# Kernel optimization log

Measured on AMD Instinct MI355X. Metric: run time of the kernel, lower is better.

## Reference

```python
import jax, jax.numpy as jnp
import numpy as np

D_MODEL = 1024
N_HEADS = 16
FEATURE_DIM = 16
HEAD_DIM = D_MODEL // N_HEADS  # 64
EPS = 1e-12


def taylor_exp(x):
    """2nd-order Taylor feature map of exp(q^T k / sqrt(d)).
    x: (b, h, l, d) -> (b, h, l, 1 + d + d^2)"""
    d = x.shape[-1]
    rd = jnp.sqrt(jnp.asarray(d, x.dtype))      # sqrt(d)
    rrd = jnp.sqrt(rd)                          # d^(1/4)
    r2 = jnp.sqrt(jnp.asarray(2.0, x.dtype))
    x2 = (x[..., :, None] * x[..., None, :]).reshape(*x.shape[:-1], d * d) / r2
    ones = jnp.ones_like(x[..., :1])
    return jnp.concatenate([ones, x / rrd, x2 / rd], axis=-1)


def setup_inputs() -> dict:
    key = jax.random.key(0)
    k0, k1, k2, k3, k4 = jax.random.split(key, 5)
    b, l = 1, 1024
    scale = 1.0 / np.sqrt(D_MODEL)
    hidden_states = jax.random.normal(k0, (b, l, D_MODEL), dtype=jnp.float32)
    Wq = jax.random.normal(k1, (N_HEADS * FEATURE_DIM, D_MODEL), dtype=jnp.float32) * scale
    Wk = jax.random.normal(k2, (N_HEADS * FEATURE_DIM, D_MODEL), dtype=jnp.float32) * scale
    Wv = jax.random.normal(k3, (N_HEADS * HEAD_DIM, D_MODEL), dtype=jnp.float32) * scale
    Wo = jax.random.normal(k4, (D_MODEL, N_HEADS * HEAD_DIM), dtype=jnp.float32) * scale
    return {"hidden_states": hidden_states, "Wq": Wq, "Wk": Wk, "Wv": Wv, "Wo": Wo}


def reference(hidden_states, Wq, Wk, Wv, Wo):
    b, l, _ = hidden_states.shape
    # projections (bias-free)
    q = (hidden_states @ Wq.T).reshape(b, l, N_HEADS, FEATURE_DIM).transpose(0, 2, 1, 3)
    k = (hidden_states @ Wk.T).reshape(b, l, N_HEADS, FEATURE_DIM).transpose(0, 2, 1, 3)
    v = (hidden_states @ Wv.T).reshape(b, l, N_HEADS, HEAD_DIM).transpose(0, 2, 1, 3)
    qf = taylor_exp(q)   # (b, h, l, D) with D = 1 + d + d^2 = 273
    kf = taylor_exp(k)
    # causal linear attention via associative KV accumulation
    # kv_state[l] = sum_{t<=l} phi(k_t) outer v_t  -> (b, h, l, head_dim, D)
    kv_state = jnp.cumsum(kf[..., None, :] * v[..., :, None], axis=2)
    num = jnp.einsum('bhlD,bhldD->bhld', qf, kv_state)
    den = jnp.einsum('bhlD,bhlD->bhl', qf, jnp.cumsum(kf, axis=2))[..., None] + EPS
    y = num / den                                # (b, h, l, head_dim)
    y = y.transpose(0, 2, 1, 3).reshape(b, l, N_HEADS * HEAD_DIM)
    return y @ Wo.T
```

## Files before the change

### kernel.cpp

```cpp
#include <hip/hip_runtime.h>

#define LSEQ 1024
#define DMODEL 1024
#define NHEADS 16
#define FDIM 16
#define HDIM 64
#define CHUNK 64
#define NCHUNK 16

typedef __attribute__((ext_vector_type(8))) short short8;
typedef __attribute__((ext_vector_type(4))) float floatx4;

__device__ __forceinline__ float bf2f(unsigned short u) {
    unsigned int x = ((unsigned int)u) << 16;
    return __builtin_bit_cast(float, x);
}
__device__ __forceinline__ unsigned short f2bf(float f) {
    unsigned int x = __builtin_bit_cast(unsigned int, f);
    unsigned int r = (x + 0x7fffu + ((x >> 16) & 1u)) >> 16;
    return (unsigned short)r;
}

__device__ __forceinline__ int block_detect_fp32(const unsigned short* wq) {
    __shared__ int cnt;
    if (threadIdx.x == 0) cnt = 0;
    __syncthreads();
    int bad = 0;
    for (int i = threadIdx.x; i < 1024; i += blockDim.x) {
        int e = (wq[i] >> 7) & 0xFF;
        if (e >= 143 || (e > 0 && e <= 80)) bad++;
    }
    if (bad) atomicAdd(&cnt, bad);
    __syncthreads();
    return cnt > 128;
}

#define U_QB   0
#define U_KB   262144
#define U_VB   524288
#define U_YB   1572864

#define MFMA(a, b, c) __builtin_amdgcn_mfma_f32_16x16x32_bf16((a), (b), (c), 0, 0, 0)

__device__ __forceinline__ void gemm64_body(
    unsigned short (&As)[64][136], unsigned short (&Bs)[64][136],
    const void* Araw, int a_fp32, int arow0,
    const void* Braw, int b_fp32, int brow0, floatx4 acc[4]) {
    int t = threadIdx.x;
    int r = t >> 2, c0 = (t & 3) * 32;
    int wave = t >> 6, lane = t & 63;
    int ml = lane & 15, q4 = lane >> 4;
    int mq = (wave >> 1) * 32, nq = (wave & 1) * 32;
    #pragma unroll
    for (int i = 0; i < 4; ++i) acc[i] = (floatx4){0.f, 0.f, 0.f, 0.f};

    short8 av[4], bv[4], av2[4], bv2[4];
    auto stage = [&](int k0, short8* a, short8* b) {
        if (!a_fp32) {
            const unsigned short* Ap = (const unsigned short*)Araw + (size_t)(arow0 + r) * DMODEL + k0 + c0;
            #pragma unroll
            for (int j = 0; j < 4; ++j) a[j] = *(const short8*)(Ap + j * 8);
        } else {
            const float* Ap = (const float*)Araw + (size_t)(arow0 + r) * DMODEL + k0 + c0;
            #pragma unroll
            for (int j = 0; j < 4; ++j)
                #pragma unroll
                for (int u = 0; u < 8; ++u) a[j][u] = (short)f2bf(Ap[j * 8 + u]);
        }
        if (!b_fp32) {
            const unsigned short* Bp = (const unsigned short*)Braw + (size_t)(brow0 + r) * DMODEL + k0 + c0;
            #pragma unroll
            for (int j = 0; j < 4; ++j) b[j] = *(const short8*)(Bp + j * 8);
        } else {
            const float* Bp = (const float*)Braw + (size_t)(brow0 + r) * DMODEL + k0 + c0;
            #pragma unroll
            for (int j = 0; j < 4; ++j)
                #pragma unroll
                for (int u = 0; u < 8; ++u) b[j][u] = (short)f2bf(Bp[j * 8 + u]);
        }
    };

    stage(0, av, bv);
    for (int k0 = 0; k0 < DMODEL; k0 += 128) {
        __syncthreads();
        #pragma unroll
        for (int j = 0; j < 4; ++j) {
            *(short8*)&As[r][c0 + j * 8] = av[j];
            *(short8*)&Bs[r][c0 + j * 8] = bv[j];
        }
        __syncthreads();
        if (k0 + 128 < DMODEL) stage(k0 + 128, av2, bv2);
        #pragma unroll
        for (int kk = 0; kk < 4; ++kk) {
            short8 a0 = *(const short8*)&As[mq + ml][kk * 32 + q4 * 8];
            short8 a1 = *(const short8*)&As[mq + 16 + ml][kk * 32 + q4 * 8];
            short8 b0 = *(const short8*)&Bs[nq + ml][kk * 32 + q4 * 8];
            short8 b1 = *(const short8*)&Bs[nq + 16 + ml][kk * 32 + q4 * 8];
            acc[0] = MFMA(a0, b0, acc[0]); acc[1] = MFMA(a0, b1, acc[1]);
            acc[2] = MFMA(a1, b0, acc[2]); acc[3] = MFMA(a1, b1, acc[3]);
        }
        #pragma unroll
        for (int j = 0; j < 4; ++j) { av[j] = av2[j]; bv[j] = bv2[j]; }
    }
}

__global__ __launch_bounds__(256) void qkv_gemm(
    const void* __restrict__ hidR, const void* __restrict__ WqR,
    const void* __restrict__ WkR, const void* __restrict__ WvR,
    unsigned short* __restrict__ qb, unsigned short* __restrict__ kb,
    unsigned short* __restrict__ vb) {
    int fp32 = block_detect_fp32((const unsigned short*)WqR);
    __shared__ __align__(16) unsigned short As[64][136];
    __shared__ __align__(16) unsigned short Bs[64][136];
    int nb = blockIdx.x, mb = blockIdx.y;
    const void* Braw; unsigned short* Cout; int ldc, col0, br0;
    if (nb < 4)      { Braw = WqR; br0 = nb * 64;       Cout = qb; ldc = 256;  col0 = nb * 64; }
    else if (nb < 8) { Braw = WkR; br0 = (nb - 4) * 64; Cout = kb; ldc = 256;  col0 = (nb - 4) * 64; }
    else             { Braw = WvR; br0 = (nb - 8) * 64; Cout = vb; ldc = 1024; col0 = (nb - 8) * 64; }

    floatx4 acc[4];
    gemm64_body(As, Bs, hidR, fp32, mb * 64, Braw, fp32, br0, acc);

    int wave = threadIdx.x >> 6, lane = threadIdx.x & 63;
    int ml = lane & 15, q4 = lane >> 4;
    int mq = (wave >> 1) * 32, nq = (wave & 1) * 32;
    #pragma unroll
    for (int mi = 0; mi < 2; ++mi)
        #pragma unroll
        for (int ni = 0; ni < 2; ++ni) {
            floatx4 a = acc[mi * 2 + ni];
            int nloc = nq + ni * 16 + ml;
            #pragma unroll
            for (int r4 = 0; r4 < 4; ++r4) {
                int row = mb * 64 + mq + mi * 16 + q4 * 4 + r4;
                Cout[(size_t)row * ldc + col0 + nloc] = f2bf(a[r4]);
            }
        }
}

__global__ __launch_bounds__(256) void flash_attn(
    const unsigned short* __restrict__ qb, const unsigned short* __restrict__ kb,
    const unsigned short* __restrict__ vb, unsigned short* __restrict__ ybB) {
    int h = blockIdx.x & 15, c = blockIdx.x >> 4;
    int l0 = c * CHUNK;
    __shared__ __align__(16) unsigned short qs[64][40];
    __shared__ __align__(16) unsigned short ksm[64][40];
    __shared__ __align__(16) unsigned short vT[80][72];
    __shared__ __align__(16) unsigned short P[64][72];
    int t = threadIdx.x, lane = t & 63, wave = t >> 6;
    int ml = lane & 15, q4 = lane >> 4;
    int m0 = wave * 16;
    int sm = t >> 2, si4 = (t & 3) * 4, scc = (t & 3) * 16;

    {
        *(ushort4*)&qs[sm][si4] = *(const ushort4*)&qb[(size_t)(l0 + sm) * 256 + h * 16 + si4];
        ushort4 z = {0, 0, 0, 0};
        *(ushort4*)&qs[sm][16 + si4]  = z;
        *(ushort4*)&ksm[sm][16 + si4] = z;
    }
    if (t < 64) {
        vT[64][t] = 0x3F80;
        #pragma unroll
        for (int i = 65; i < 80; ++i) vT[i][t] = 0;
    }

    auto load_kv = [&](int j, ushort4& kr, ushort4 vr[4]) {
        kr = *(const ushort4*)&kb[(size_t)(j * 64 + sm) * 256 + h * 16 + si4];
        #pragma unroll
        for (int u = 0; u < 4; ++u)
            vr[u] = *(const ushort4*)&vb[(size_t)(j * 64 + sm) * 1024 + h * 64 + scc + u * 4];
    };

    floatx4 acc[5];
    #pragma unroll
    for (int i = 0; i < 5; ++i) acc[i] = (floatx4){0.f, 0.f, 0.f, 0.f};

    ushort4 kr, vr[4], kr2, vr2[4];
    load_kv(0, kr, vr);

    for (int j = 0; j <= c; ++j) {
        {
            *(ushort4*)&ksm[sm][si4] = kr;
            unsigned short tmp[16];
            #pragma unroll
            for (int u = 0; u < 4; ++u) *(ushort4*)&tmp[u * 4] = vr[u];
            #pragma unroll
            for (int u = 0; u < 16; ++u) vT[scc + u][sm] = tmp[u];
        }
        __syncthreads();
        if (j < c) load_kv(j + 1, kr2, vr2);

        short8 aq = *(const short8*)&qs[m0 + ml][q4 * 8];
        bool diag = (j == c);
        #pragma unroll
        for (int nt = 0; nt < 4; ++nt) {
            short8 bk = *(const short8*)&ksm[nt * 16 + ml][q4 * 8];
            floatx4 s4 = {0.f, 0.f, 0.f, 0.f};
            s4 = MFMA(aq, bk, s4);
            int tt = nt * 16 + ml;
            #pragma unroll
            for (int r = 0; r < 4; ++r) {
                int lrow = m0 + q4 * 4 + r;
                float s = s4[r];
                float p = 1.f + 0.25f * s + 0.03125f * s * s;
                if (diag && tt > lrow) p = 0.f;
                P[lrow][tt] = f2bf(p);
            }
        }

        #pragma unroll
        for (int k0 = 0; k0 < 64; k0 += 32) {
            short8 ap = *(const short8*)&P[m0 + ml][k0 + q4 * 8];
            #pragma unroll
            for (int nt = 0; nt < 5; ++nt) {
                short8 bvv = *(const short8*)&vT[nt * 16 + ml][k0 + q4 * 8];
                acc[nt] = MFMA(ap, bvv, acc[nt]);
            }
        }
        __syncthreads();
        kr = kr2;
        #pragma unroll
        for (int u = 0; u < 4; ++u) vr[u] = vr2[u];
    }

    #pragma unroll
    for (int r = 0; r < 4; ++r) {
        float den = __shfl(acc[4][r], q4 * 16) + 1e-12f;
        float dinv = 1.f / den;
        int lrow = m0 + q4 * 4 + r;
        unsigned short* yp = ybB + (size_t)(l0 + lrow) * 1024 + h * 64;
        #pragma unroll
        for (int nt = 0; nt < 4; ++nt)
            yp[nt * 16 + ml] = f2bf(acc[nt][r] * dinv);
    }
}

__global__ __launch_bounds__(256) void out_gemm(
    const unsigned short* __restrict__ A, const void* __restrict__ WoR,
    void* __restrict__ outv, const unsigned short* __restrict__ wqraw) {
    int fp32 = block_detect_fp32(wqraw);
    __shared__ __align__(16) unsigned short As[64][136];
    __shared__ __align__(16) unsigned short Bs[64][136];
    int nb = blockIdx.x, mb = blockIdx.y;

    floatx4 acc[4];
    gemm64_body(As, Bs, A, 0, mb * 64, WoR, fp32, nb * 64, acc);

    int wave = threadIdx.x >> 6, lane = threadIdx.x & 63;
    int ml = lane & 15, q4 = lane >> 4;
    int mq = (wave >> 1) * 32, nq = (wave & 1) * 32;
    #pragma unroll
    for (int mi = 0; mi < 2; ++mi)
        #pragma unroll
        for (int ni = 0; ni < 2; ++ni) {
            floatx4 a = acc[mi * 2 + ni];
            int n = nb * 64 + nq + ni * 16 + ml;
            #pragma unroll
            for (int r4 = 0; r4 < 4; ++r4) {
                int row = mb * 64 + mq + mi * 16 + q4 * 4 + r4;
                size_t idx = (size_t)row * 1024 + n;
                if (fp32) ((float*)outv)[idx] = a[r4];
                else      ((unsigned short*)outv)[idx] = f2bf(a[r4]);
            }
        }
}

extern "C" void kernel_launch(void* const* d_in, const int* in_sizes, int n_in,
                              void* d_out, int out_size, void* d_ws, size_t ws_size,
                              hipStream_t stream) {
    unsigned short* us = (unsigned short*)d_ws;
    unsigned short* qbB = us + U_QB;
    unsigned short* kbB = us + U_KB;
    unsigned short* vbB = us + U_VB;
    unsigned short* ybB = us + U_YB;
    size_t need = (size_t)(U_YB + 1048576) * 2ull;
    if (ws_size < need) return;

    qkv_gemm<<<dim3(24, 16), 256, 0, stream>>>(d_in[0], d_in[1], d_in[2], d_in[3], qbB, kbB, vbB);
    flash_attn<<<dim3(256), 256, 0, stream>>>(qbB, kbB, vbB, ybB);
    out_gemm<<<dim3(16, 16), 256, 0, stream>>>(ybB, d_in[4], d_out, (const unsigned short*)d_in[1]);
}
```

Measured before the change: 141.5 us.

## Split causal attention KV range across two blocks with atomic-flag merge

Each (head, chunk) attention tile is now computed by two blocks, each covering half of the causal KV chunks. Both blocks write partial numerators and denominators to workspace, and the last block to finish, found with an atomic counter, combines the two partials and writes the normalized output. This is meant to even out the load imbalance from the triangular causal work and to double the number of blocks on the 256-CU device. In exchange it adds fp32 partial writes and reads plus fences. The counters are reset inside the QKV GEMM kernel.

```diff
diff --git a/kernel.cpp b/kernel.cpp
--- a/kernel.cpp
+++ b/kernel.cpp
@@ -39,6 +39,7 @@
 #define U_KB   262144
 #define U_VB   524288
 #define U_YB   1572864
+#define U_END  2621440
 
 #define MFMA(a, b, c) __builtin_amdgcn_mfma_f32_16x16x32_bf16((a), (b), (c), 0, 0, 0)
 
@@ -108,7 +109,9 @@
     const void* __restrict__ hidR, const void* __restrict__ WqR,
     const void* __restrict__ WkR, const void* __restrict__ WvR,
     unsigned short* __restrict__ qb, unsigned short* __restrict__ kb,
-    unsigned short* __restrict__ vb) {
+    unsigned short* __restrict__ vb, int* __restrict__ flagW) {
+    if (blockIdx.x == 0 && blockIdx.y == 0 && threadIdx.x < 256)
+        flagW[threadIdx.x] = 0;
     int fp32 = block_detect_fp32((const unsigned short*)WqR);
     __shared__ __align__(16) unsigned short As[64][136];
     __shared__ __align__(16) unsigned short Bs[64][136];
@@ -140,13 +143,20 @@
 
 __global__ __launch_bounds__(256) void flash_attn(
     const unsigned short* __restrict__ qb, const unsigned short* __restrict__ kb,
-    const unsigned short* __restrict__ vb, unsigned short* __restrict__ ybB) {
-    int h = blockIdx.x & 15, c = blockIdx.x >> 4;
+    const unsigned short* __restrict__ vb, unsigned short* __restrict__ ybB,
+    float* __restrict__ numW, float* __restrict__ denW, int* __restrict__ flagW) {
+    int idx = blockIdx.x & 255;
+    int s = blockIdx.x >> 8;
+    int h = idx & 15, c = idx >> 4;
+    int half = (c + 1) >> 1;
+    int j0 = s ? half : 0;
+    int j1 = s ? c : half - 1;
     int l0 = c * CHUNK;
     __shared__ __align__(16) unsigned short qs[64][40];
     __shared__ __align__(16) unsigned short ksm[64][40];
     __shared__ __align__(16) unsigned short vT[80][72];
     __shared__ __align__(16) unsigned short P[64][72];
+    __shared__ int turn;
     int t = threadIdx.x, lane = t & 63, wave = t >> 6;
     int ml = lane & 15, q4 = lane >> 4;
     int m0 = wave * 16;
@@ -176,62 +186,83 @@
     for (int i = 0; i < 5; ++i) acc[i] = (floatx4){0.f, 0.f, 0.f, 0.f};
 
     ushort4 kr, vr[4], kr2, vr2[4];
-    load_kv(0, kr, vr);
-
-    for (int j = 0; j <= c; ++j) {
-        {
-            *(ushort4*)&ksm[sm][si4] = kr;
-            unsigned short tmp[16];
-            #pragma unroll
-            for (int u = 0; u < 4; ++u) *(ushort4*)&tmp[u * 4] = vr[u];
-            #pragma unroll
-            for (int u = 0; u < 16; ++u) vT[scc + u][sm] = tmp[u];
-        }
-        __syncthreads();
-        if (j < c) load_kv(j + 1, kr2, vr2);
-
-        short8 aq = *(const short8*)&qs[m0 + ml][q4 * 8];
-        bool diag = (j == c);
-        #pragma unroll
-        for (int nt = 0; nt < 4; ++nt) {
-            short8 bk = *(const short8*)&ksm[nt * 16 + ml][q4 * 8];
-            floatx4 s4 = {0.f, 0.f, 0.f, 0.f};
-            s4 = MFMA(aq, bk, s4);
-            int tt = nt * 16 + ml;
-            #pragma unroll
-            for (int r = 0; r < 4; ++r) {
-                int lrow = m0 + q4 * 4 + r;
-                float s = s4[r];
-                float p = 1.f + 0.25f * s + 0.03125f * s * s;
-                if (diag && tt > lrow) p = 0.f;
-                P[lrow][tt] = f2bf(p);
-            }
-        }
-
-        #pragma unroll
-        for (int k0 = 0; k0 < 64; k0 += 32) {
-            short8 ap = *(const short8*)&P[m0 + ml][k0 + q4 * 8];
-            #pragma unroll
-            for (int nt = 0; nt < 5; ++nt) {
-                short8 bvv = *(const short8*)&vT[nt * 16 + ml][k0 + q4 * 8];
-                acc[nt] = MFMA(ap, bvv, acc[nt]);
-            }
-        }
-        __syncthreads();
-        kr = kr2;
-        #pragma unroll
-        for (int u = 0; u < 4; ++u) vr[u] = vr2[u];
-    }
-
+    if (j0 <= j1) {
+        load_kv(j0, kr, vr);
+        for (int j = j0; j <= j1; ++j) {
+            {
+                *(ushort4*)&ksm[sm][si4] = kr;
+                unsigned short tmp[16];
+                #pragma unroll
+                for (int u = 0; u < 4; ++u) *(ushort4*)&tmp[u * 4] = vr[u];
+                #pragma unroll
+                for (int u = 0; u < 16; ++u) vT[scc + u][sm] = tmp[u];
+            }
+            __syncthreads();
+            if (j < j1) load_kv(j + 1, kr2, vr2);
+
+            short8 aq = *(const short8*)&qs[m0 + ml][q4 * 8];
+            bool diag = (j == c);
+            #pragma unroll
+            for (int nt = 0; nt < 4; ++nt) {
+                short8 bk = *(const short8*)&ksm[nt * 16 + ml][q4 * 8];
+                floatx4 s4 = {0.f, 0.f, 0.f, 0.f};
+                s4 = MFMA(aq, bk, s4);
+                int tt = nt * 16 + ml;
+                #pragma unroll
+                for (int r = 0; r < 4; ++r) {
+                    int lrow = m0 + q4 * 4 + r;
+                    float sc = s4[r];
+                    float p = 1.f + 0.25f * sc + 0.03125f * sc * sc;
+                    if (diag && tt > lrow) p = 0.f;
+                    P[lrow][tt] = f2bf(p);
+                }
+            }
+
+            #pragma unroll
+            for (int k0 = 0; k0 < 64; k0 += 32) {
+                short8 ap = *(const short8*)&P[m0 + ml][k0 + q4 * 8];
+                #pragma unroll
+                for (int nt = 0; nt < 5; ++nt) {
+                    short8 bvv = *(const short8*)&vT[nt * 16 + ml][k0 + q4 * 8];
+                    acc[nt] = MFMA(ap, bvv, acc[nt]);
+                }
+            }
+            __syncthreads();
+            kr = kr2;
+            #pragma unroll
+            for (int u = 0; u < 4; ++u) vr[u] = vr2[u];
+        }
+    }
+
+    float* np = numW + ((size_t)idx * 2 + s) * 4096;
+    #pragma unroll
+    for (int nt = 0; nt < 4; ++nt)
+        #pragma unroll
+        for (int r = 0; r < 4; ++r)
+            np[(m0 + q4 * 4 + r) * 64 + nt * 16 + ml] = acc[nt][r];
+    if (ml == 0) {
+        float* dp = denW + ((size_t)idx * 2 + s) * 64;
+        #pragma unroll
+        for (int r = 0; r < 4; ++r) dp[m0 + q4 * 4 + r] = acc[4][r];
+    }
+    __threadfence();
+    if (t == 0) turn = atomicAdd(&flagW[idx], 1);
+    __syncthreads();
+    if (turn == 0) return;
+    __threadfence();
+
+    int so = 1 - s;
+    const float* no_ = numW + ((size_t)idx * 2 + so) * 4096;
+    const float* do_ = denW + ((size_t)idx * 2 + so) * 64;
     #pragma unroll
     for (int r = 0; r < 4; ++r) {
-        float den = __shfl(acc[4][r], q4 * 16) + 1e-12f;
+        int lrow = m0 + q4 * 4 + r;
+        float den = __shfl(acc[4][r], q4 * 16) + do_[lrow] + 1e-12f;
         float dinv = 1.f / den;
-        int lrow = m0 + q4 * 4 + r;
         unsigned short* yp = ybB + (size_t)(l0 + lrow) * 1024 + h * 64;
         #pragma unroll
         for (int nt = 0; nt < 4; ++nt)
-            yp[nt * 16 + ml] = f2bf(acc[nt][r] * dinv);
+            yp[nt * 16 + ml] = f2bf((acc[nt][r] + no_[lrow * 64 + nt * 16 + ml]) * dinv);
     }
 }
 
@@ -273,10 +304,14 @@
     unsigned short* kbB = us + U_KB;
     unsigned short* vbB = us + U_VB;
     unsigned short* ybB = us + U_YB;
-    size_t need = (size_t)(U_YB + 1048576) * 2ull;
+    float* fws  = (float*)(us + U_END);
+    float* numW = fws;
+    float* denW = fws + 2097152;
+    int*   flagW = (int*)(denW + 32768);
+    size_t need = (size_t)U_END * 2ull + (size_t)(2097152 + 32768 + 256) * 4ull;
     if (ws_size < need) return;
 
-    qkv_gemm<<<dim3(24, 16), 256, 0, stream>>>(d_in[0], d_in[1], d_in[2], d_in[3], qbB, kbB, vbB);
-    flash_attn<<<dim3(256), 256, 0, stream>>>(qbB, kbB, vbB, ybB);
+    qkv_gemm<<<dim3(24, 16), 256, 0, stream>>>(d_in[0], d_in[1], d_in[2], d_in[3], qbB, kbB, vbB, flagW);
+    flash_attn<<<dim3(512), 256, 0, stream>>>(qbB, kbB, vbB, ybB, numW, denW, flagW);
     out_gemm<<<dim3(16, 16), 256, 0, stream>>>(ybB, d_in[4], d_out, (const unsigned short*)d_in[1]);
 }
```

Result: slower. 220.3 us (+55.6%).
